# Kernel tuning notes

Measured on AMD Instinct MI355X. Metric: run time of the kernel, lower is better.

## Reference

```python
import jax, jax.numpy as jnp
import numpy as np

TAU = 2.0
V_TH = 1.0
V_RESET = 0.0


def setup_inputs() -> dict:
    key = jax.random.key(0)
    k1, k2 = jax.random.split(key)
    T, N, C, H, W = 16, 8, 64, 64, 64
    x_seq = jax.random.normal(k1, (T, N, C, H, W), dtype=jnp.float32)
    conv_weight = jax.random.normal(k2, (C, C, 3, 3), dtype=jnp.float32) * 0.05
    return {"x_seq": x_seq, "conv_weight": conv_weight}


def _conv2d(x, w):
    # x: (B, C, H, W), w: (Cout, Cin, 3, 3), padding=1, no bias
    return jax.lax.conv_general_dilated(
        x, w, window_strides=(1, 1), padding=((1, 1), (1, 1)),
        dimension_numbers=("NCHW", "OIHW", "NCHW"))


def _lif_scan(z_seq):
    # z_seq: (T, N, C, H, W); LIF: decay_input=True, hard reset to V_RESET.
    def step(v, x):
        # charge: v = v + (x - (v - v_reset)) / tau
        v = v + (x - (v - V_RESET)) / TAU
        s = (v >= V_TH).astype(v.dtype)
        # hard reset: v = (1 - s) * v + s * v_reset
        v = (1.0 - s) * v + s * V_RESET
        return v, s

    v0 = jnp.full(z_seq.shape[1:], V_RESET, dtype=z_seq.dtype)
    _, spikes = jax.lax.scan(step, v0, z_seq)
    return spikes


def reference(x_seq, conv_weight):
    T, N = x_seq.shape[:2]
    z = _conv2d(x_seq.reshape(T * N, *x_seq.shape[2:]), conv_weight)
    z = z.reshape(T, N, *z.shape[1:])
    return _lif_scan(z)
```

## Files before the change

### kernel.cpp

```cpp
#include <hip/hip_runtime.h>


namespace {
constexpr int T = 16, N = 8, C = 64, H = 64, W = 64;
constexpr int HW   = H * W;
constexpr int CHW  = C * HW;
constexpr int NCHW = N * CHW;
constexpr int NWT  = C * C * 9;
constexpr int NPOS = 10 * 18;
}

__global__ void wtr_kernel(const float* __restrict__ w, float* __restrict__ wt2) {
    int i = blockIdx.x * 256 + threadIdx.x;
    if (i >= NWT) return;
    int tap  = i % 9;
    int rem  = i / 9;
    int ci   = rem % 64;
    int cout = rem / 64;
    wt2[(tap * 64 + ci) * 64 + cout] = w[i];
}

__global__ __launch_bounds__(256, 3) void conv_kernel(
    const float* __restrict__ x,
    const float* __restrict__ wt2,
    float*       __restrict__ zo)
{
#pragma clang fp contract(off)
    __shared__ float xs[16 * NPOS * 4];

    const int tid  = threadIdx.x;
    const int wave = __builtin_amdgcn_readfirstlane(tid >> 6);
    const int lane = tid & 63;
    const int px = lane & 7;
    const int py = lane >> 3;
    const int c0 = wave << 4;

    const int bid  = blockIdx.x;
    const int t    = bid >> 8;
    const int r    = bid & 255;
    const int n    = r >> 5;
    const int tile = r & 31;
    const int th0 = (tile >> 2) << 3;
    const int tw0 = (tile & 3) << 4;

    const float* xt = x + (size_t)(t * N + n) * CHW;

#pragma unroll
    for (int it = 0; it < 45; ++it) {
        int j  = tid + it * 256;
        int ci = j / NPOS;
        int rr = j - ci * NPOS;
        int dy = rr / 18;
        int dx = rr - dy * 18;
        int hh = th0 - 1 + dy;
        int ww = tw0 - 1 + dx;
        float val = 0.0f;
        if ((unsigned)hh < (unsigned)H && (unsigned)ww < (unsigned)W)
            val = xt[ci * HW + hh * W + ww];
        xs[(ci >> 2) * (NPOS * 4) + rr * 4 + (ci & 3)] = val;
    }
    __syncthreads();

    float acc0[16], acc1[16];
#pragma unroll
    for (int i = 0; i < 16; ++i) { acc0[i] = 0.0f; acc1[i] = 0.0f; }

    for (int tap = 0; tap < 9; ++tap) {
        const int ky = tap / 3, kx = tap - 3 * ky;
        const int pos = (py + ky) * 18 + (px + kx);
        const float4* xp = (const float4*)xs + pos;
        const float* wtap = wt2 + tap * 4096 + c0;
#pragma unroll 2
        for (int cib = 0; cib < 16; ++cib) {
            const float4 xv0 = xp[cib * NPOS];
            const float4 xv1 = xp[cib * NPOS + 8];
            const float* wp = wtap + cib * 256;
#pragma unroll
            for (int cc = 0; cc < 16; ++cc) {
                float w0 = wp[cc];
                acc0[cc] = fmaf(w0, xv0.x, acc0[cc]);
                acc1[cc] = fmaf(w0, xv1.x, acc1[cc]);
            }
#pragma unroll
            for (int cc = 0; cc < 16; ++cc) {
                float w1 = wp[64 + cc];
                acc0[cc] = fmaf(w1, xv0.y, acc0[cc]);
                acc1[cc] = fmaf(w1, xv1.y, acc1[cc]);
            }
#pragma unroll
            for (int cc = 0; cc < 16; ++cc) {
                float w2 = wp[128 + cc];
                acc0[cc] = fmaf(w2, xv0.z, acc0[cc]);
                acc1[cc] = fmaf(w2, xv1.z, acc1[cc]);
            }
#pragma unroll
            for (int cc = 0; cc < 16; ++cc) {
                float w3 = wp[192 + cc];
                acc0[cc] = fmaf(w3, xv0.w, acc0[cc]);
                acc1[cc] = fmaf(w3, xv1.w, acc1[cc]);
            }
        }
    }

    float* zt = zo + (size_t)(t * N + n) * CHW;
    const int pbase = (th0 + py) * W + (tw0 + px);
#pragma unroll
    for (int cc = 0; cc < 16; ++cc) {
        zt[(c0 + cc) * HW + pbase]     = acc0[cc];
        zt[(c0 + cc) * HW + pbase + 8] = acc1[cc];
    }
}

__global__ void lif_kernel(float* __restrict__ zo) {
#pragma clang fp contract(off)
    const int gid = blockIdx.x * 256 + threadIdx.x;
    float4 v;
    v.x = 0.0f; v.y = 0.0f; v.z = 0.0f; v.w = 0.0f;
#pragma unroll
    for (int t = 0; t < T; ++t) {
        float4* p = (float4*)(zo + (size_t)t * NCHW) + gid;
        float4 z = *p;
        float4 s;
#define LIF_STEP(comp) { float d = z.comp - v.comp; float hh = d * 0.5f;      \
        v.comp = v.comp + hh;                                                  \
        if (v.comp >= 1.0f) { s.comp = 1.0f; v.comp = 0.0f; }                  \
        else                { s.comp = 0.0f; } }
        LIF_STEP(x) LIF_STEP(y) LIF_STEP(z) LIF_STEP(w)
#undef LIF_STEP
        *p = s;
    }
}

extern "C" void kernel_launch(void* const* d_in, const int* in_sizes, int n_in,
                              void* d_out, int out_size, void* d_ws, size_t ws_size,
                              hipStream_t stream) {
    const float* x = (const float*)d_in[0];
    const float* w = (const float*)d_in[1];
    if (n_in >= 2 && in_sizes[0] < in_sizes[1]) {
        const float* tmp = x; x = w; w = tmp;
    }
    float* out = (float*)d_out;
    float* wt2 = (float*)d_ws;

    wtr_kernel<<<(NWT + 255) / 256, 256, 0, stream>>>(w, wt2);
    conv_kernel<<<T * N * 32, 256, 0, stream>>>(x, wt2, out);
    lif_kernel<<<NCHW / 1024, 256, 0, stream>>>(out);
}
```

Baseline: 629.8 us.

## Add large-tile conv kernel with 16x32 tiles and 64 outputs per thread

Adds a conv kernel that gives each 512-thread block a 16x32 output tile for all 64 channels, with a 156 KB dynamic LDS halo buffer. Each thread now holds four 16-channel accumulator sets, so every weight load feeds four FMAs instead of two, and the halo overhead per output shrinks. The launcher opts into the large shared-memory size once and falls back to the old kernel if that call fails. In exchange, only one block fits per CU. The halo load phase can then no longer overlap another block's compute, and there are fewer waves to hide latency.

```diff
diff --git a/kernel.cpp b/kernel.cpp
--- a/kernel.cpp
+++ b/kernel.cpp
@@ -8,6 +8,8 @@
 constexpr int NCHW = N * CHW;
 constexpr int NWT  = C * C * 9;
 constexpr int NPOS = 10 * 18;
+constexpr int BPOS = 18 * 34;
+constexpr int BLDS = 16 * BPOS * 16;
 }
 
 __global__ void wtr_kernel(const float* __restrict__ w, float* __restrict__ wt2) {
@@ -18,6 +20,114 @@
     int ci   = rem % 64;
     int cout = rem / 64;
     wt2[(tap * 64 + ci) * 64 + cout] = w[i];
+}
+
+__global__ __launch_bounds__(512) void conv_big(
+    const float* __restrict__ x,
+    const float* __restrict__ wt2,
+    float*       __restrict__ zo)
+{
+#pragma clang fp contract(off)
+    extern __shared__ float xs[];
+
+    const int tid  = threadIdx.x;
+    const int wave = __builtin_amdgcn_readfirstlane(tid >> 6);
+    const int lane = tid & 63;
+    const int px = lane & 7;
+    const int py = lane >> 3;
+    const int c0  = (wave & 3) << 4;
+    const int row = ((wave >> 2) << 3) + py;
+
+    const int bid  = blockIdx.x;
+    const int t    = bid >> 6;
+    const int r    = bid & 63;
+    const int n    = r >> 3;
+    const int tile = r & 7;
+    const int th0 = (tile >> 1) << 4;
+    const int tw0 = (tile & 1) << 5;
+
+    const float* xt = x + (size_t)(t * N + n) * CHW;
+
+#pragma unroll
+    for (int it = 0; it < 77; ++it) {
+        int j = tid + it * 512;
+        if (j < 64 * BPOS) {
+            int ci = j / BPOS;
+            int rr = j - ci * BPOS;
+            int dy = rr / 34;
+            int dx = rr - dy * 34;
+            int hh = th0 - 1 + dy;
+            int ww = tw0 - 1 + dx;
+            float val = 0.0f;
+            if ((unsigned)hh < (unsigned)H && (unsigned)ww < (unsigned)W)
+                val = xt[ci * HW + hh * W + ww];
+            xs[(ci >> 2) * (BPOS * 4) + rr * 4 + (ci & 3)] = val;
+        }
+    }
+    __syncthreads();
+
+    float acc0[16], acc1[16], acc2[16], acc3[16];
+#pragma unroll
+    for (int i = 0; i < 16; ++i) {
+        acc0[i] = 0.0f; acc1[i] = 0.0f; acc2[i] = 0.0f; acc3[i] = 0.0f;
+    }
+
+    for (int tap = 0; tap < 9; ++tap) {
+        const int ky = tap / 3, kx = tap - 3 * ky;
+        const int pos = (row + ky) * 34 + (px + kx);
+        const float4* xp = (const float4*)xs + pos;
+        const float* wtap = wt2 + tap * 4096 + c0;
+#pragma unroll 2
+        for (int cib = 0; cib < 16; ++cib) {
+            const float4 xv0 = xp[cib * BPOS];
+            const float4 xv1 = xp[cib * BPOS + 8];
+            const float4 xv2 = xp[cib * BPOS + 16];
+            const float4 xv3 = xp[cib * BPOS + 24];
+            const float* wp = wtap + cib * 256;
+#pragma unroll
+            for (int cc = 0; cc < 16; ++cc) {
+                float w0 = wp[cc];
+                acc0[cc] = fmaf(w0, xv0.x, acc0[cc]);
+                acc1[cc] = fmaf(w0, xv1.x, acc1[cc]);
+                acc2[cc] = fmaf(w0, xv2.x, acc2[cc]);
+                acc3[cc] = fmaf(w0, xv3.x, acc3[cc]);
+            }
+#pragma unroll
+            for (int cc = 0; cc < 16; ++cc) {
+                float w1 = wp[64 + cc];
+                acc0[cc] = fmaf(w1, xv0.y, acc0[cc]);
+                acc1[cc] = fmaf(w1, xv1.y, acc1[cc]);
+                acc2[cc] = fmaf(w1, xv2.y, acc2[cc]);
+                acc3[cc] = fmaf(w1, xv3.y, acc3[cc]);
+            }
+#pragma unroll
+            for (int cc = 0; cc < 16; ++cc) {
+                float w2 = wp[128 + cc];
+                acc0[cc] = fmaf(w2, xv0.z, acc0[cc]);
+                acc1[cc] = fmaf(w2, xv1.z, acc1[cc]);
+                acc2[cc] = fmaf(w2, xv2.z, acc2[cc]);
+                acc3[cc] = fmaf(w2, xv3.z, acc3[cc]);
+            }
+#pragma unroll
+            for (int cc = 0; cc < 16; ++cc) {
+                float w3 = wp[192 + cc];
+                acc0[cc] = fmaf(w3, xv0.w, acc0[cc]);
+                acc1[cc] = fmaf(w3, xv1.w, acc1[cc]);
+                acc2[cc] = fmaf(w3, xv2.w, acc2[cc]);
+                acc3[cc] = fmaf(w3, xv3.w, acc3[cc]);
+            }
+        }
+    }
+
+    float* zt = zo + (size_t)(t * N + n) * CHW;
+    const int pbase = (th0 + row) * W + (tw0 + px);
+#pragma unroll
+    for (int cc = 0; cc < 16; ++cc) {
+        zt[(c0 + cc) * HW + pbase]      = acc0[cc];
+        zt[(c0 + cc) * HW + pbase + 8]  = acc1[cc];
+        zt[(c0 + cc) * HW + pbase + 16] = acc2[cc];
+        zt[(c0 + cc) * HW + pbase + 24] = acc3[cc];
+    }
 }
 
 __global__ __launch_bounds__(256, 3) void conv_kernel(
@@ -142,7 +252,19 @@
     float* out = (float*)d_out;
     float* wt2 = (float*)d_ws;
 
+    static int big_ok = -1;
+    if (big_ok < 0) {
+        hipError_t e = hipFuncSetAttribute(
+            reinterpret_cast<const void*>(&conv_big),
+            hipFuncAttributeMaxDynamicSharedMemorySize, BLDS);
+        big_ok = (e == hipSuccess) ? 1 : 0;
+        (void)hipGetLastError();
+    }
+
     wtr_kernel<<<(NWT + 255) / 256, 256, 0, stream>>>(w, wt2);
-    conv_kernel<<<T * N * 32, 256, 0, stream>>>(x, wt2, out);
+    if (big_ok)
+        conv_big<<<T * N * 8, 512, BLDS, stream>>>(x, wt2, out);
+    else
+        conv_kernel<<<T * N * 32, 256, 0, stream>>>(x, wt2, out);
     lif_kernel<<<NCHW / 1024, 256, 0, stream>>>(out);
 }
```

Result: slower. 759.0 us (+20.5%).
